# Optimization experiments

Hardware: AMD Instinct MI355X
Metric: run time of the kernel (lower is better)

Reference implementation:

```python
import jax, jax.numpy as jnp
import numpy as np


def _dwconv(x, w, pad):
    # depthwise conv, NCHW, weight (C,1,kh,kw), feature_group_count=C
    return jax.lax.conv_general_dilated(
        x, w, window_strides=(1, 1), padding=pad,
        feature_group_count=x.shape[1],
        dimension_numbers=('NCHW', 'OIHW', 'NCHW'))


def _max_channel_relu(x):
    # assumed MaxChannelReLU: keep only the channel-max value at each (b,h,w)
    return x * (x == jnp.max(x, axis=1, keepdims=True))


def setup_inputs() -> dict:
    key = jax.random.key(0)
    ks = jax.random.split(key, 6)
    B, C, H, W = 16, 64, 128, 128
    x = jax.random.normal(ks[0], (B, C, H, W), dtype=jnp.float32)
    w_bbx = 0.1 * jax.random.normal(ks[1], (C, 1, 1, 1), dtype=jnp.float32)
    w_width = 0.1 * jax.random.normal(ks[2], (C, 1, 1, 11), dtype=jnp.float32)
    w_width_sh = 0.1 * jax.random.normal(ks[3], (C, 1, 1, 1), dtype=jnp.float32)
    w_height = 0.1 * jax.random.normal(ks[4], (C, 1, 11, 1), dtype=jnp.float32)
    w_height_sh = 0.1 * jax.random.normal(ks[5], (C, 1, 1, 1), dtype=jnp.float32)
    return {"x": x, "w_bbx": w_bbx, "w_width": w_width,
            "w_width_sh": w_width_sh, "w_height": w_height,
            "w_height_sh": w_height_sh}


def reference(x, w_bbx, w_width, w_width_sh, w_height, w_height_sh):
    B, C, H, W = x.shape
    # self.bbx: depthwise 1x1 conv == per-channel scale
    wh = x * w_bbx.reshape(1, C, 1, 1)
    # width branch: depthwise (1,11) conv pad 5, scaled by W, then shared 1x1
    w = _dwconv(wh, w_width, [(0, 0), (5, 5)]) * W
    w = w * w_width_sh.reshape(1, C, 1, 1)
    # height branch: depthwise (11,1) conv pad 5, scaled by H, then shared 1x1
    h = _dwconv(wh, w_height, [(5, 5), (0, 0)]) * H
    h = h * w_height_sh.reshape(1, C, 1, 1)
    sx = jax.nn.sigmoid(x)
    M = jnp.max(sx, axis=(-2, -1), keepdims=True) - 0.01
    score = x * (sx > M).astype(x.dtype)
    S = jnp.sum(score, axis=(-2, -1), keepdims=True)
    sn = score / S  # normalized weights, reused by all weighted reductions
    ws = jnp.sum(w * sn, axis=(-2, -1))
    hs = jnp.sum(h * sn, axis=(-2, -1))
    ps = jnp.max(sx, axis=(-2, -1))
    col = jnp.arange(W, dtype=x.dtype).reshape(1, 1, 1, W)
    row = jnp.arange(H, dtype=x.dtype).reshape(1, 1, H, 1)
    x1 = jnp.sum(col * sn, axis=(-2, -1)) - ws / 2
    y1 = jnp.sum(row * sn, axis=(-2, -1)) - hs / 2
    x2 = x1 + ws
    y2 = y1 + hs
    score_m = _max_channel_relu(score)
    w_m = _max_channel_relu(w)
    h_m = _max_channel_relu(h)
    i = jnp.broadcast_to(jnp.arange(B, dtype=x.dtype)[:, None], (B, C))
    bbox = jnp.stack([i, x1, y1, x2, y2, ps], axis=-1).reshape(-1, 6)
    return jnp.concatenate([score_m, w_m, h_m], axis=1), bbox
```

## Files before the change

### kernel.cpp

```cpp
#include <hip/hip_runtime.h>
#include <math.h>

#define BATCH 16
#define CH    64
#define HH    128
#define WW    128
#define PLANE (HH*WW)
#define OUT0  (BATCH*3*CH*PLANE)
#define BP    (BATCH*PLANE)

#define T_OFF   0
#define PS_OFF  1024
#define SUM_OFF 2048
#define CW_OFF  12288
#define CHS_OFF 12352
#define MAP_OFF 16384
#define FMAP_OFF 3163136

__device__ __forceinline__ void conv4(const float* __restrict__ base,
                                      const float* __restrict__ wk,
                                      const float* __restrict__ hk,
                                      float cw, float chs, float T,
                                      float4& w4, float4& h4, float4& s4) {
    float4 vx;
    float hx = 0.f, hy = 0.f, hz = 0.f, hw = 0.f;
#pragma unroll
    for (int k = 0; k < 11; k++) {
        float4 v = *(const float4*)(base + k * 144 + 8);
        if (k == 5) vx = v;
        hx = fmaf(v.x, hk[k], hx);
        hy = fmaf(v.y, hk[k], hy);
        hz = fmaf(v.z, hk[k], hz);
        hw = fmaf(v.w, hk[k], hw);
    }
    float wbuf[20];
    {
        float4 a0 = *(const float4*)(base + 5 * 144 + 0);
        float4 a1 = *(const float4*)(base + 5 * 144 + 4);
        float4 a3 = *(const float4*)(base + 5 * 144 + 12);
        float4 a4 = *(const float4*)(base + 5 * 144 + 16);
        wbuf[0] = a0.x;  wbuf[1] = a0.y;  wbuf[2] = a0.z;  wbuf[3] = a0.w;
        wbuf[4] = a1.x;  wbuf[5] = a1.y;  wbuf[6] = a1.z;  wbuf[7] = a1.w;
        wbuf[8] = vx.x;  wbuf[9] = vx.y;  wbuf[10] = vx.z; wbuf[11] = vx.w;
        wbuf[12] = a3.x; wbuf[13] = a3.y; wbuf[14] = a3.z; wbuf[15] = a3.w;
        wbuf[16] = a4.x; wbuf[17] = a4.y; wbuf[18] = a4.z; wbuf[19] = a4.w;
    }
    float wo[4];
#pragma unroll
    for (int j = 0; j < 4; j++) {
        float acc = 0.f;
#pragma unroll
        for (int k = 0; k < 11; k++) acc = fmaf(wbuf[j + 3 + k], wk[k], acc);
        wo[j] = acc * cw;
    }
    w4.x = wo[0]; w4.y = wo[1]; w4.z = wo[2]; w4.w = wo[3];
    h4.x = hx * chs; h4.y = hy * chs; h4.z = hz * chs; h4.w = hw * chs;
    s4.x = (vx.x > T) ? vx.x : 0.f;
    s4.y = (vx.y > T) ? vx.y : 0.f;
    s4.z = (vx.z > T) ? vx.z : 0.f;
    s4.w = (vx.w > T) ? vx.w : 0.f;
}

__global__ __launch_bounds__(256) void k_max(const float* __restrict__ x,
                                             const float* __restrict__ w_bbx,
                                             const float* __restrict__ w_width_sh,
                                             const float* __restrict__ w_height_sh,
                                             float* __restrict__ ws) {
    int bid = blockIdx.x;
    const float4* xp = (const float4*)(x + (size_t)bid * PLANE);
    int tid = threadIdx.x;
    float m = -INFINITY;
#pragma unroll
    for (int i = 0; i < 16; i++) {
        float4 v = xp[i * 256 + tid];
        m = fmaxf(m, fmaxf(fmaxf(v.x, v.y), fmaxf(v.z, v.w)));
    }
#pragma unroll
    for (int off = 32; off; off >>= 1) m = fmaxf(m, __shfl_xor(m, off, 64));
    __shared__ float sm[4];
    int wid = tid >> 6, lane = tid & 63;
    if (lane == 0) sm[wid] = m;
    __syncthreads();
    if (tid == 0) {
        float mm = fmaxf(fmaxf(sm[0], sm[1]), fmaxf(sm[2], sm[3]));
        float ps = 1.0f / (1.0f + expf(-mm));
        float M = ps - 0.01f;
        float T = (M > 0.0f) ? logf(M / (1.0f - M)) : -INFINITY;
        ws[T_OFF + bid] = T;
        ws[PS_OFF + bid] = ps;
    }
    if (bid < 64 && tid == 1) {
        float cb = w_bbx[bid];
        ws[CW_OFF + bid]  = 128.0f * w_width_sh[bid] * cb;
        ws[CHS_OFF + bid] = 128.0f * w_height_sh[bid] * cb;
    }
}

__global__ __launch_bounds__(256) void k_cmax(const float* __restrict__ x,
                                              const float* __restrict__ w_width,
                                              const float* __restrict__ w_height,
                                              float* __restrict__ ws) {
    __shared__ float4 xs4[4 * 18 * 36];
    float* xs = (float*)xs4;
    int bid = blockIdx.x;
    int cg   = bid & 3;
    int band = (bid >> 2) & 15;
    int b    = bid >> 6;
    int r0 = band * 8;
    int tid = threadIdx.x;

    for (int i = tid; i < 4 * 18 * 36; i += 256)
        xs4[i] = make_float4(0.f, 0.f, 0.f, 0.f);

    int lr_o = tid >> 5;
    int c0 = (tid & 31) << 2;

    float4 mw = make_float4(-INFINITY, -INFINITY, -INFINITY, -INFINITY);
    float4 mh = mw, ms = mw;

    for (int chunk = 0; chunk < 4; chunk++) {
        int ch0 = cg * 16 + chunk * 4;
        __syncthreads();
        for (int j = tid; j < 4 * 576; j += 256) {
            int i = j / 576;
            int rem = j - i * 576;
            int lr = rem >> 5;
            int c4 = rem & 31;
            int gr = r0 - 5 + lr;
            if (gr >= 0 && gr < 128) {
                float4 v = *(const float4*)(x +
                    ((size_t)((b * 64 + ch0 + i) * 128 + gr)) * 128 + c4 * 4);
                *(float4*)(xs + (i * 18 + lr) * 144 + 8 + c4 * 4) = v;
            }
        }
        __syncthreads();
#pragma unroll
        for (int i = 0; i < 4; i++) {
            int c = ch0 + i;
            float T   = ws[T_OFF + b * 64 + c];
            float cw  = ws[CW_OFF + c];
            float chs = ws[CHS_OFF + c];
            float wk[11], hk[11];
#pragma unroll
            for (int k = 0; k < 11; k++) {
                wk[k] = w_width[c * 11 + k];
                hk[k] = w_height[c * 11 + k];
            }
            float4 w4, h4, s4;
            conv4(xs + (i * 18 + lr_o) * 144 + c0, wk, hk, cw, chs, T, w4, h4, s4);
            mw.x = fmaxf(mw.x, w4.x); mw.y = fmaxf(mw.y, w4.y);
            mw.z = fmaxf(mw.z, w4.z); mw.w = fmaxf(mw.w, w4.w);
            mh.x = fmaxf(mh.x, h4.x); mh.y = fmaxf(mh.y, h4.y);
            mh.z = fmaxf(mh.z, h4.z); mh.w = fmaxf(mh.w, h4.w);
            ms.x = fmaxf(ms.x, s4.x); ms.y = fmaxf(ms.y, s4.y);
            ms.z = fmaxf(ms.z, s4.z); ms.w = fmaxf(ms.w, s4.w);
        }
    }
    int p = b * PLANE + (r0 + lr_o) * 128 + c0;
    *(float4*)(ws + MAP_OFF + (size_t)(cg * 3 + 0) * BP + p) = mw;
    *(float4*)(ws + MAP_OFF + (size_t)(cg * 3 + 1) * BP + p) = mh;
    *(float4*)(ws + MAP_OFF + (size_t)(cg * 3 + 2) * BP + p) = ms;
}

__global__ __launch_bounds__(256) void k_combine(float* __restrict__ ws) {
    int id = blockIdx.x * 256 + threadIdx.x;
    int f = id >> 16;
    int r = id & 65535;
    float4 m = *(const float4*)(ws + MAP_OFF + (size_t)f * BP + (size_t)r * 4);
#pragma unroll
    for (int g = 1; g < 4; g++) {
        float4 v = *(const float4*)(ws + MAP_OFF + (size_t)(g * 3 + f) * BP + (size_t)r * 4);
        m.x = fmaxf(m.x, v.x); m.y = fmaxf(m.y, v.y);
        m.z = fmaxf(m.z, v.z); m.w = fmaxf(m.w, v.w);
    }
    *(float4*)(ws + FMAP_OFF + (size_t)f * BP + (size_t)r * 4) = m;
}

__global__ __launch_bounds__(256) void k_write(
    const float* __restrict__ x,
    const float* __restrict__ w_width, const float* __restrict__ w_height,
    float* __restrict__ ws, float* __restrict__ out) {
    __shared__ float xs[74 * 144];
    __shared__ float red[4 * 5];
    int bid = blockIdx.x;
    int half = bid & 1;
    int plane = bid >> 1;
    int b = plane >> 6, c = plane & 63;
    int r0 = half * 64;
    int tid = threadIdx.x;

    float4* xs4 = (float4*)xs;
    for (int i = tid; i < 74 * 36; i += 256) xs4[i] = make_float4(0.f, 0.f, 0.f, 0.f);
    __syncthreads();
    const float* xp = x + (size_t)plane * PLANE;
    for (int j = tid; j < 74 * 32; j += 256) {
        int br = j >> 5, c4 = j & 31;
        int gr = r0 - 5 + br;
        if (gr >= 0 && gr < 128)
            *(float4*)&xs[br * 144 + 8 + c4 * 4] =
                *(const float4*)(xp + gr * 128 + c4 * 4);
    }
    float wk[11], hk[11];
#pragma unroll
    for (int k = 0; k < 11; k++) {
        wk[k] = w_width[c * 11 + k];
        hk[k] = w_height[c * 11 + k];
    }
    float T   = ws[T_OFF + plane];
    float cw  = ws[CW_OFF + c];
    float chs = ws[CHS_OFF + c];
    __syncthreads();

    float S = 0.f, Sw = 0.f, Sh = 0.f, Scol = 0.f, Srow = 0.f;
    float* outS = out + (size_t)(b * 192 + c) * PLANE + r0 * 128;
    float* outW = out + (size_t)(b * 192 + 64 + c) * PLANE + r0 * 128;
    float* outH = out + (size_t)(b * 192 + 128 + c) * PLANE + r0 * 128;
    const float* mwp = ws + FMAP_OFF + 0 * (size_t)BP + b * PLANE + r0 * 128;
    const float* mhp = ws + FMAP_OFF + 1 * (size_t)BP + b * PLANE + r0 * 128;
    const float* msp = ws + FMAP_OFF + 2 * (size_t)BP + b * PLANE + r0 * 128;

    for (int g = 0; g < 8; g++) {
        int idx = g * 256 + tid;
        int p = idx * 4;
        int y = p >> 7, xc = p & 127;
        float4 w4, h4, s4;
        conv4(xs + y * 144 + xc, wk, hk, cw, chs, T, w4, h4, s4);

        float s4sum = s4.x + s4.y + s4.z + s4.w;
        S += s4sum;
        Srow += (float)(r0 + y) * s4sum;
        Sw = fmaf(w4.x, s4.x, Sw); Sw = fmaf(w4.y, s4.y, Sw);
        Sw = fmaf(w4.z, s4.z, Sw); Sw = fmaf(w4.w, s4.w, Sw);
        Sh = fmaf(h4.x, s4.x, Sh); Sh = fmaf(h4.y, s4.y, Sh);
        Sh = fmaf(h4.z, s4.z, Sh); Sh = fmaf(h4.w, s4.w, Sh);
        Scol = fmaf((float)(xc + 0), s4.x, Scol);
        Scol = fmaf((float)(xc + 1), s4.y, Scol);
        Scol = fmaf((float)(xc + 2), s4.z, Scol);
        Scol = fmaf((float)(xc + 3), s4.w, Scol);

        float4 mw = *(const float4*)(mwp + p);
        float4 mh = *(const float4*)(mhp + p);
        float4 ms = *(const float4*)(msp + p);
        float4 o;
        o.x = (s4.x == ms.x) ? s4.x : 0.f;
        o.y = (s4.y == ms.y) ? s4.y : 0.f;
        o.z = (s4.z == ms.z) ? s4.z : 0.f;
        o.w = (s4.w == ms.w) ? s4.w : 0.f;
        ((float4*)outS)[idx] = o;
        o.x = (w4.x == mw.x) ? w4.x : 0.f;
        o.y = (w4.y == mw.y) ? w4.y : 0.f;
        o.z = (w4.z == mw.z) ? w4.z : 0.f;
        o.w = (w4.w == mw.w) ? w4.w : 0.f;
        ((float4*)outW)[idx] = o;
        o.x = (h4.x == mh.x) ? h4.x : 0.f;
        o.y = (h4.y == mh.y) ? h4.y : 0.f;
        o.z = (h4.z == mh.z) ? h4.z : 0.f;
        o.w = (h4.w == mh.w) ? h4.w : 0.f;
        ((float4*)outH)[idx] = o;
    }
#pragma unroll
    for (int off = 32; off; off >>= 1) {
        S    += __shfl_xor(S, off, 64);
        Sw   += __shfl_xor(Sw, off, 64);
        Sh   += __shfl_xor(Sh, off, 64);
        Scol += __shfl_xor(Scol, off, 64);
        Srow += __shfl_xor(Srow, off, 64);
    }
    int wid = tid >> 6, lane = tid & 63;
    if (lane == 0) {
        red[wid * 5 + 0] = S;   red[wid * 5 + 1] = Sw;
        red[wid * 5 + 2] = Sh;  red[wid * 5 + 3] = Scol;
        red[wid * 5 + 4] = Srow;
    }
    __syncthreads();
    if (tid == 0) {
        float a0 = 0, a1 = 0, a2 = 0, a3 = 0, a4 = 0;
#pragma unroll
        for (int w2 = 0; w2 < 4; w2++) {
            a0 += red[w2 * 5 + 0]; a1 += red[w2 * 5 + 1];
            a2 += red[w2 * 5 + 2]; a3 += red[w2 * 5 + 3];
            a4 += red[w2 * 5 + 4];
        }
        int base = SUM_OFF + half * 5120;
        ws[base + 0 * 1024 + plane] = a0;
        ws[base + 1 * 1024 + plane] = a1;
        ws[base + 2 * 1024 + plane] = a2;
        ws[base + 3 * 1024 + plane] = a3;
        ws[base + 4 * 1024 + plane] = a4;
    }
}

__global__ __launch_bounds__(256) void k_bbox(const float* __restrict__ ws,
                                              float* __restrict__ out) {
    int idx = blockIdx.x * 256 + threadIdx.x;
    if (idx >= 1024) return;
    int b = idx >> 6;
    float S    = ws[SUM_OFF + 0 * 1024 + idx] + ws[SUM_OFF + 5120 + 0 * 1024 + idx];
    float Sw   = ws[SUM_OFF + 1 * 1024 + idx] + ws[SUM_OFF + 5120 + 1 * 1024 + idx];
    float Sh   = ws[SUM_OFF + 2 * 1024 + idx] + ws[SUM_OFF + 5120 + 2 * 1024 + idx];
    float Scol = ws[SUM_OFF + 3 * 1024 + idx] + ws[SUM_OFF + 5120 + 3 * 1024 + idx];
    float Srow = ws[SUM_OFF + 4 * 1024 + idx] + ws[SUM_OFF + 5120 + 4 * 1024 + idx];
    float ps   = ws[PS_OFF + idx];
    float inv = 1.0f / S;
    float wsv = Sw * inv, hsv = Sh * inv;
    float x1 = Scol * inv - 0.5f * wsv;
    float y1 = Srow * inv - 0.5f * hsv;
    float* o = out + OUT0 + (size_t)idx * 6;
    o[0] = (float)b;
    o[1] = x1;
    o[2] = y1;
    o[3] = x1 + wsv;
    o[4] = y1 + hsv;
    o[5] = ps;
}

extern "C" void kernel_launch(void* const* d_in, const int* in_sizes, int n_in,
                              void* d_out, int out_size, void* d_ws, size_t ws_size,
                              hipStream_t stream) {
    const float* x          = (const float*)d_in[0];
    const float* w_bbx      = (const float*)d_in[1];
    const float* w_width    = (const float*)d_in[2];
    const float* w_width_sh = (const float*)d_in[3];
    const float* w_height   = (const float*)d_in[4];
    const float* w_height_sh= (const float*)d_in[5];
    float* out = (float*)d_out;
    float* ws  = (float*)d_ws;

    k_max<<<dim3(1024), dim3(256), 0, stream>>>(x, w_bbx, w_width_sh, w_height_sh, ws);
    k_cmax<<<dim3(1024), dim3(256), 0, stream>>>(x, w_width, w_height, ws);
    k_combine<<<dim3(768), dim3(256), 0, stream>>>(ws);
    k_write<<<dim3(2048), dim3(256), 0, stream>>>(x, w_width, w_height, ws, out);
    k_bbox<<<dim3(4), dim3(256), 0, stream>>>(ws, out);
}
```

Before: 318.1 us.

## Compute vertical conv over row strips with register ring buffer reuse

Adds a conv_strip helper in which each thread computes several consecutive output rows and keeps the 11-row vertical window in a register ring buffer, so each new row costs one shared-memory load instead of eleven. In k_cmax each wave now handles one channel over a 4-row strip, and the per-channel maxima are merged across waves through shared memory before a single write. Block ordering also changes so bands are the fastest-varying index. k_write uses 8-row strips per thread. This trades LDS traffic for more registers (ring buffer plus per-row accumulators), which may lower occupancy.

Result: no change. 323.8 us (+1.8%).

```diff
diff --git a/kernel.cpp b/kernel.cpp
--- a/kernel.cpp
+++ b/kernel.cpp
@@ -17,48 +17,67 @@
 #define MAP_OFF 16384
 #define FMAP_OFF 3163136
 
-__device__ __forceinline__ void conv4(const float* __restrict__ base,
-                                      const float* __restrict__ wk,
-                                      const float* __restrict__ hk,
-                                      float cw, float chs, float T,
-                                      float4& w4, float4& h4, float4& s4) {
-    float4 vx;
-    float hx = 0.f, hy = 0.f, hz = 0.f, hw = 0.f;
-#pragma unroll
-    for (int k = 0; k < 11; k++) {
-        float4 v = *(const float4*)(base + k * 144 + 8);
-        if (k == 5) vx = v;
-        hx = fmaf(v.x, hk[k], hx);
-        hy = fmaf(v.y, hk[k], hy);
-        hz = fmaf(v.z, hk[k], hz);
-        hw = fmaf(v.w, hk[k], hw);
-    }
-    float wbuf[20];
-    {
-        float4 a0 = *(const float4*)(base + 5 * 144 + 0);
-        float4 a1 = *(const float4*)(base + 5 * 144 + 4);
-        float4 a3 = *(const float4*)(base + 5 * 144 + 12);
-        float4 a4 = *(const float4*)(base + 5 * 144 + 16);
-        wbuf[0] = a0.x;  wbuf[1] = a0.y;  wbuf[2] = a0.z;  wbuf[3] = a0.w;
-        wbuf[4] = a1.x;  wbuf[5] = a1.y;  wbuf[6] = a1.z;  wbuf[7] = a1.w;
-        wbuf[8] = vx.x;  wbuf[9] = vx.y;  wbuf[10] = vx.z; wbuf[11] = vx.w;
-        wbuf[12] = a3.x; wbuf[13] = a3.y; wbuf[14] = a3.z; wbuf[15] = a3.w;
-        wbuf[16] = a4.x; wbuf[17] = a4.y; wbuf[18] = a4.z; wbuf[19] = a4.w;
-    }
-    float wo[4];
-#pragma unroll
-    for (int j = 0; j < 4; j++) {
-        float acc = 0.f;
-#pragma unroll
-        for (int k = 0; k < 11; k++) acc = fmaf(wbuf[j + 3 + k], wk[k], acc);
-        wo[j] = acc * cw;
-    }
-    w4.x = wo[0]; w4.y = wo[1]; w4.z = wo[2]; w4.w = wo[3];
-    h4.x = hx * chs; h4.y = hy * chs; h4.z = hz * chs; h4.w = hw * chs;
-    s4.x = (vx.x > T) ? vx.x : 0.f;
-    s4.y = (vx.y > T) ? vx.y : 0.f;
-    s4.z = (vx.z > T) ? vx.z : 0.f;
-    s4.w = (vx.w > T) ? vx.w : 0.f;
+__device__ __forceinline__ float4 fmax4(float4 a, float4 b) {
+    float4 r;
+    r.x = fmaxf(a.x, b.x); r.y = fmaxf(a.y, b.y);
+    r.z = fmaxf(a.z, b.z); r.w = fmaxf(a.w, b.w);
+    return r;
+}
+
+template <int ROWS, class F>
+__device__ __forceinline__ void conv_strip(const float* __restrict__ base,
+                                           const float* __restrict__ wk,
+                                           const float* __restrict__ hk,
+                                           float cw, float chs, float T,
+                                           F&& emit) {
+    float4 rb[11];
+#pragma unroll
+    for (int r = 0; r < 11; r++)
+        rb[r] = *(const float4*)(base + r * 144 + 8);
+#pragma unroll
+    for (int j = 0; j < ROWS; j++) {
+        if (j > 0)
+            rb[(j + 10) % 11] = *(const float4*)(base + (j + 10) * 144 + 8);
+        float hx = 0.f, hy = 0.f, hz = 0.f, hw = 0.f;
+#pragma unroll
+        for (int k = 0; k < 11; k++) {
+            float4 v = rb[(j + k) % 11];
+            hx = fmaf(v.x, hk[k], hx);
+            hy = fmaf(v.y, hk[k], hy);
+            hz = fmaf(v.z, hk[k], hz);
+            hw = fmaf(v.w, hk[k], hw);
+        }
+        float4 vx = rb[(j + 5) % 11];
+        float wbuf[20];
+        {
+            const float* row = base + (j + 5) * 144;
+            float4 a0 = *(const float4*)(row + 0);
+            float4 a1 = *(const float4*)(row + 4);
+            float4 a3 = *(const float4*)(row + 12);
+            float4 a4 = *(const float4*)(row + 16);
+            wbuf[0] = a0.x;  wbuf[1] = a0.y;  wbuf[2] = a0.z;  wbuf[3] = a0.w;
+            wbuf[4] = a1.x;  wbuf[5] = a1.y;  wbuf[6] = a1.z;  wbuf[7] = a1.w;
+            wbuf[8] = vx.x;  wbuf[9] = vx.y;  wbuf[10] = vx.z; wbuf[11] = vx.w;
+            wbuf[12] = a3.x; wbuf[13] = a3.y; wbuf[14] = a3.z; wbuf[15] = a3.w;
+            wbuf[16] = a4.x; wbuf[17] = a4.y; wbuf[18] = a4.z; wbuf[19] = a4.w;
+        }
+        float wo[4];
+#pragma unroll
+        for (int q = 0; q < 4; q++) {
+            float acc = 0.f;
+#pragma unroll
+            for (int k = 0; k < 11; k++) acc = fmaf(wbuf[q + 3 + k], wk[k], acc);
+            wo[q] = acc * cw;
+        }
+        float4 w4, h4, s4;
+        w4.x = wo[0]; w4.y = wo[1]; w4.z = wo[2]; w4.w = wo[3];
+        h4.x = hx * chs; h4.y = hy * chs; h4.z = hz * chs; h4.w = hw * chs;
+        s4.x = (vx.x > T) ? vx.x : 0.f;
+        s4.y = (vx.y > T) ? vx.y : 0.f;
+        s4.z = (vx.z > T) ? vx.z : 0.f;
+        s4.w = (vx.w > T) ? vx.w : 0.f;
+        emit(j, w4, h4, s4);
+    }
 }
 
 __global__ __launch_bounds__(256) void k_max(const float* __restrict__ x,
@@ -100,23 +119,29 @@
                                               const float* __restrict__ w_width,
                                               const float* __restrict__ w_height,
                                               float* __restrict__ ws) {
-    __shared__ float4 xs4[4 * 18 * 36];
-    float* xs = (float*)xs4;
+    __shared__ float xs[4 * 18 * 144];
     int bid = blockIdx.x;
-    int cg   = bid & 3;
-    int band = (bid >> 2) & 15;
+    int band = bid & 15;
+    int cg   = (bid >> 4) & 3;
     int b    = bid >> 6;
     int r0 = band * 8;
     int tid = threadIdx.x;
-
+    int cs = tid & 31;
+    int rs = (tid >> 5) & 1;
+    int ig = tid >> 6;
+    int slot = tid & 63;
+
+    float4* xs4 = (float4*)xs;
     for (int i = tid; i < 4 * 18 * 36; i += 256)
         xs4[i] = make_float4(0.f, 0.f, 0.f, 0.f);
 
-    int lr_o = tid >> 5;
-    int c0 = (tid & 31) << 2;
-
-    float4 mw = make_float4(-INFINITY, -INFINITY, -INFINITY, -INFINITY);
-    float4 mh = mw, ms = mw;
+    float4 mw[4], mh[4], ms[4];
+#pragma unroll
+    for (int j = 0; j < 4; j++) {
+        mw[j] = make_float4(-INFINITY, -INFINITY, -INFINITY, -INFINITY);
+        mh[j] = mw[j];
+        ms[j] = mw[j];
+    }
 
     for (int chunk = 0; chunk < 4; chunk++) {
         int ch0 = cg * 16 + chunk * 4;
@@ -127,39 +152,59 @@
             int lr = rem >> 5;
             int c4 = rem & 31;
             int gr = r0 - 5 + lr;
-            if (gr >= 0 && gr < 128) {
-                float4 v = *(const float4*)(x +
-                    ((size_t)((b * 64 + ch0 + i) * 128 + gr)) * 128 + c4 * 4);
-                *(float4*)(xs + (i * 18 + lr) * 144 + 8 + c4 * 4) = v;
+            if (gr >= 0 && gr < 128)
+                *(float4*)(xs + (i * 18 + lr) * 144 + 8 + c4 * 4) =
+                    *(const float4*)(x +
+                        ((size_t)((b * 64 + ch0 + i) * 128 + gr)) * 128 + c4 * 4);
+        }
+        __syncthreads();
+        int c = ch0 + ig;
+        float T   = ws[T_OFF + b * 64 + c];
+        float cwv = ws[CW_OFF + c];
+        float chsv= ws[CHS_OFF + c];
+        float wk[11], hk[11];
+#pragma unroll
+        for (int k = 0; k < 11; k++) {
+            wk[k] = w_width[c * 11 + k];
+            hk[k] = w_height[c * 11 + k];
+        }
+        const float* basep = xs + (ig * 18 + rs * 4) * 144 + cs * 4;
+        conv_strip<4>(basep, wk, hk, cwv, chsv, T,
+            [&](int j, float4 w4, float4 h4, float4 s4) {
+                mw[j] = fmax4(mw[j], w4);
+                mh[j] = fmax4(mh[j], h4);
+                ms[j] = fmax4(ms[j], s4);
+            });
+    }
+    __syncthreads();
+    float4* cb = (float4*)xs;
+    if (ig > 0) {
+#pragma unroll
+        for (int j = 0; j < 4; j++) {
+            cb[((ig - 1) * 64 + slot) * 12 + j]     = mw[j];
+            cb[((ig - 1) * 64 + slot) * 12 + 4 + j] = mh[j];
+            cb[((ig - 1) * 64 + slot) * 12 + 8 + j] = ms[j];
+        }
+    }
+    __syncthreads();
+    if (ig == 0) {
+#pragma unroll
+        for (int g = 0; g < 3; g++) {
+#pragma unroll
+            for (int j = 0; j < 4; j++) {
+                mw[j] = fmax4(mw[j], cb[(g * 64 + slot) * 12 + j]);
+                mh[j] = fmax4(mh[j], cb[(g * 64 + slot) * 12 + 4 + j]);
+                ms[j] = fmax4(ms[j], cb[(g * 64 + slot) * 12 + 8 + j]);
             }
         }
-        __syncthreads();
-#pragma unroll
-        for (int i = 0; i < 4; i++) {
-            int c = ch0 + i;
-            float T   = ws[T_OFF + b * 64 + c];
-            float cw  = ws[CW_OFF + c];
-            float chs = ws[CHS_OFF + c];
-            float wk[11], hk[11];
-#pragma unroll
-            for (int k = 0; k < 11; k++) {
-                wk[k] = w_width[c * 11 + k];
-                hk[k] = w_height[c * 11 + k];
-            }
-            float4 w4, h4, s4;
-            conv4(xs + (i * 18 + lr_o) * 144 + c0, wk, hk, cw, chs, T, w4, h4, s4);
-            mw.x = fmaxf(mw.x, w4.x); mw.y = fmaxf(mw.y, w4.y);
-            mw.z = fmaxf(mw.z, w4.z); mw.w = fmaxf(mw.w, w4.w);
-            mh.x = fmaxf(mh.x, h4.x); mh.y = fmaxf(mh.y, h4.y);
-            mh.z = fmaxf(mh.z, h4.z); mh.w = fmaxf(mh.w, h4.w);
-            ms.x = fmaxf(ms.x, s4.x); ms.y = fmaxf(ms.y, s4.y);
-            ms.z = fmaxf(ms.z, s4.z); ms.w = fmaxf(ms.w, s4.w);
-        }
-    }
-    int p = b * PLANE + (r0 + lr_o) * 128 + c0;
-    *(float4*)(ws + MAP_OFF + (size_t)(cg * 3 + 0) * BP + p) = mw;
-    *(float4*)(ws + MAP_OFF + (size_t)(cg * 3 + 1) * BP + p) = mh;
-    *(float4*)(ws + MAP_OFF + (size_t)(cg * 3 + 2) * BP + p) = ms;
+        int pbase = b * PLANE + (r0 + rs * 4) * 128 + cs * 4;
+#pragma unroll
+        for (int j = 0; j < 4; j++) {
+            *(float4*)(ws + MAP_OFF + (size_t)(cg * 3 + 0) * BP + pbase + j * 128) = mw[j];
+            *(float4*)(ws + MAP_OFF + (size_t)(cg * 3 + 1) * BP + pbase + j * 128) = mh[j];
+            *(float4*)(ws + MAP_OFF + (size_t)(cg * 3 + 2) * BP + pbase + j * 128) = ms[j];
+        }
+    }
 }
 
 __global__ __launch_bounds__(256) void k_combine(float* __restrict__ ws) {
@@ -170,8 +215,7 @@
 #pragma unroll
     for (int g = 1; g < 4; g++) {
         float4 v = *(const float4*)(ws + MAP_OFF + (size_t)(g * 3 + f) * BP + (size_t)r * 4);
-        m.x = fmaxf(m.x, v.x); m.y = fmaxf(m.y, v.y);
-        m.z = fmaxf(m.z, v.z); m.w = fmaxf(m.w, v.w);
+        m = fmax4(m, v);
     }
     *(float4*)(ws + FMAP_OFF + (size_t)f * BP + (size_t)r * 4) = m;
 }
@@ -188,6 +232,8 @@
     int b = plane >> 6, c = plane & 63;
     int r0 = half * 64;
     int tid = threadIdx.x;
+    int cs = tid & 31;
+    int rs = tid >> 5;
 
     float4* xs4 = (float4*)xs;
     for (int i = tid; i < 74 * 36; i += 256) xs4[i] = make_float4(0.f, 0.f, 0.f, 0.f);
@@ -207,8 +253,8 @@
         hk[k] = w_height[c * 11 + k];
     }
     float T   = ws[T_OFF + plane];
-    float cw  = ws[CW_OFF + c];
-    float chs = ws[CHS_OFF + c];
+    float cwv = ws[CW_OFF + c];
+    float chsv= ws[CHS_OFF + c];
     __syncthreads();
 
     float S = 0.f, Sw = 0.f, Sh = 0.f, Scol = 0.f, Srow = 0.f;
@@ -219,45 +265,44 @@
     const float* mhp = ws + FMAP_OFF + 1 * (size_t)BP + b * PLANE + r0 * 128;
     const float* msp = ws + FMAP_OFF + 2 * (size_t)BP + b * PLANE + r0 * 128;
 
-    for (int g = 0; g < 8; g++) {
-        int idx = g * 256 + tid;
-        int p = idx * 4;
-        int y = p >> 7, xc = p & 127;
-        float4 w4, h4, s4;
-        conv4(xs + y * 144 + xc, wk, hk, cw, chs, T, w4, h4, s4);
-
-        float s4sum = s4.x + s4.y + s4.z + s4.w;
-        S += s4sum;
-        Srow += (float)(r0 + y) * s4sum;
-        Sw = fmaf(w4.x, s4.x, Sw); Sw = fmaf(w4.y, s4.y, Sw);
-        Sw = fmaf(w4.z, s4.z, Sw); Sw = fmaf(w4.w, s4.w, Sw);
-        Sh = fmaf(h4.x, s4.x, Sh); Sh = fmaf(h4.y, s4.y, Sh);
-        Sh = fmaf(h4.z, s4.z, Sh); Sh = fmaf(h4.w, s4.w, Sh);
-        Scol = fmaf((float)(xc + 0), s4.x, Scol);
-        Scol = fmaf((float)(xc + 1), s4.y, Scol);
-        Scol = fmaf((float)(xc + 2), s4.z, Scol);
-        Scol = fmaf((float)(xc + 3), s4.w, Scol);
-
-        float4 mw = *(const float4*)(mwp + p);
-        float4 mh = *(const float4*)(mhp + p);
-        float4 ms = *(const float4*)(msp + p);
-        float4 o;
-        o.x = (s4.x == ms.x) ? s4.x : 0.f;
-        o.y = (s4.y == ms.y) ? s4.y : 0.f;
-        o.z = (s4.z == ms.z) ? s4.z : 0.f;
-        o.w = (s4.w == ms.w) ? s4.w : 0.f;
-        ((float4*)outS)[idx] = o;
-        o.x = (w4.x == mw.x) ? w4.x : 0.f;
-        o.y = (w4.y == mw.y) ? w4.y : 0.f;
-        o.z = (w4.z == mw.z) ? w4.z : 0.f;
-        o.w = (w4.w == mw.w) ? w4.w : 0.f;
-        ((float4*)outW)[idx] = o;
-        o.x = (h4.x == mh.x) ? h4.x : 0.f;
-        o.y = (h4.y == mh.y) ? h4.y : 0.f;
-        o.z = (h4.z == mh.z) ? h4.z : 0.f;
-        o.w = (h4.w == mh.w) ? h4.w : 0.f;
-        ((float4*)outH)[idx] = o;
-    }
+    const float* basep = xs + (rs * 8) * 144 + cs * 4;
+    conv_strip<8>(basep, wk, hk, cwv, chsv, T,
+        [&](int j, float4 w4, float4 h4, float4 s4) {
+            int ly = rs * 8 + j;
+            int p = ly * 128 + cs * 4;
+            float s4sum = s4.x + s4.y + s4.z + s4.w;
+            S += s4sum;
+            Srow += (float)(r0 + ly) * s4sum;
+            Sw = fmaf(w4.x, s4.x, Sw); Sw = fmaf(w4.y, s4.y, Sw);
+            Sw = fmaf(w4.z, s4.z, Sw); Sw = fmaf(w4.w, s4.w, Sw);
+            Sh = fmaf(h4.x, s4.x, Sh); Sh = fmaf(h4.y, s4.y, Sh);
+            Sh = fmaf(h4.z, s4.z, Sh); Sh = fmaf(h4.w, s4.w, Sh);
+            int xc = cs * 4;
+            Scol = fmaf((float)(xc + 0), s4.x, Scol);
+            Scol = fmaf((float)(xc + 1), s4.y, Scol);
+            Scol = fmaf((float)(xc + 2), s4.z, Scol);
+            Scol = fmaf((float)(xc + 3), s4.w, Scol);
+
+            float4 mw = *(const float4*)(mwp + p);
+            float4 mh = *(const float4*)(mhp + p);
+            float4 msv = *(const float4*)(msp + p);
+            float4 o;
+            o.x = (s4.x == msv.x) ? s4.x : 0.f;
+            o.y = (s4.y == msv.y) ? s4.y : 0.f;
+            o.z = (s4.z == msv.z) ? s4.z : 0.f;
+            o.w = (s4.w == msv.w) ? s4.w : 0.f;
+            *(float4*)(outS + p) = o;
+            o.x = (w4.x == mw.x) ? w4.x : 0.f;
+            o.y = (w4.y == mw.y) ? w4.y : 0.f;
+            o.z = (w4.z == mw.z) ? w4.z : 0.f;
+            o.w = (w4.w == mw.w) ? w4.w : 0.f;
+            *(float4*)(outW + p) = o;
+            o.x = (h4.x == mh.x) ? h4.x : 0.f;
+            o.y = (h4.y == mh.y) ? h4.y : 0.f;
+            o.z = (h4.z == mh.z) ? h4.z : 0.f;
+            o.w = (h4.w == mh.w) ? h4.w : 0.f;
+            *(float4*)(outH + p) = o;
+        });
 #pragma unroll
     for (int off = 32; off; off >>= 1) {
         S    += __shfl_xor(S, off, 64);
```
